# Performance work log

Measured on AMD Instinct MI355X. Metric: run time of the kernel, lower is better.

Reference implementation:

```python
import jax, jax.numpy as jnp
import numpy as np

HEADS = 8

def _rotate_every_two(t):
    # t: [..., d]; interleaved rotation (-x2, x1) pairs
    x1 = t[..., ::2]
    x2 = t[..., 1::2]
    return jnp.stack([-x2, x1], axis=-1).reshape(t.shape)

def _theta_shift(t, sin, cos):
    return t * cos + _rotate_every_two(t) * sin

def setup_inputs() -> dict:
    key = jax.random.key(0)
    ks = jax.random.split(key, 5)
    B, H, W, C = 4, 40, 40, 512
    dh = C // HEADS
    x = jax.random.normal(ks[0], (B, H, W, C), dtype=jnp.float32)
    sin = jax.random.normal(ks[1], (H, W, dh), dtype=jnp.float32)
    cos = jax.random.normal(ks[2], (H, W, dh), dtype=jnp.float32)
    # 1x1 conv weight [3C, C] (kernel dims squeezed) + bias
    w_qkv = jax.random.normal(ks[3], (3 * C, C), dtype=jnp.float32) * (C ** -0.5)
    b_qkv = jnp.zeros((3 * C,), dtype=jnp.float32)
    return {"x": x, "sin": sin, "cos": cos, "w_qkv": w_qkv, "b_qkv": b_qkv}

def reference(x, sin, cos, w_qkv, b_qkv):
    B, H, W, C = x.shape
    heads = HEADS
    dh = C // heads
    scale = dh ** -0.5
    # 1x1 conv == per-pixel linear projection
    qkv = jnp.einsum('bhwc,oc->bhwo', x, w_qkv) + b_qkv  # [B,H,W,3C]
    q, k, v = jnp.split(qkv, 3, axis=-1)

    def to_heads(t):
        # channel order is (heads, dim_head) per the torch rearrange
        return t.reshape(B, H, W, heads, dh).transpose(0, 3, 1, 2, 4)  # [B,heads,H,W,dh]

    q = _theta_shift(to_heads(q), sin, cos)
    k = _theta_shift(to_heads(k), sin, cos)
    # v is computed but unused downstream in the original module (bug preserved)

    N = H * W
    q = q.reshape(B, heads, N, dh)
    k = k.reshape(B, heads, N, dh)

    attn = jnp.einsum('bhnd,bhmd->bhnm', q, k) * scale  # [B,heads,N,N]
    p = jax.nn.softmax(attn, axis=-1)
    # NOTE: original code does matmul(logist, kfine_heads) — K, not V. Kept faithful.
    out = jnp.einsum('bhnm,bhmd->bhnd', p, k)  # [B,heads,N,dh]
    out = out.transpose(0, 2, 1, 3).reshape(B, H, W, C)
    return out
```

## Files before the change

### kernel.cpp

```cpp
#include <hip/hip_runtime.h>
#include <hip/hip_bf16.h>


typedef __hip_bfloat16 bf16;
typedef __attribute__((ext_vector_type(8))) short short8;
typedef __attribute__((ext_vector_type(4))) short bfx4;
typedef __attribute__((ext_vector_type(4))) float f32x4;

#define NSP 1600
#define CDIM 512
#define DH 64

#define GLD16(g, l)                                                           \
  __builtin_amdgcn_global_load_lds(                                           \
      (const __attribute__((address_space(1))) unsigned int*)(g),             \
      (__attribute__((address_space(3))) unsigned int*)(l), 16, 0, 0)

__device__ __forceinline__ f32x4 mfma32(short8 a, short8 b, f32x4 c) {
  return __builtin_amdgcn_mfma_f32_16x16x32_bf16(a, b, c, 0, 0, 0);
}

#if __has_builtin(__builtin_amdgcn_mfma_f32_16x16x16bf16_1k)
__device__ __forceinline__ f32x4 mfma_k16(bfx4 a, bfx4 b, f32x4 c) {
  return __builtin_amdgcn_mfma_f32_16x16x16bf16_1k(a, b, c, 0, 0, 0);
}
#else
__device__ __forceinline__ f32x4 mfma_k16(bfx4 a, bfx4 b, f32x4 c) {
  short8 a8 = {a.x, a.y, a.z, a.w, 0, 0, 0, 0};
  short8 b8 = {b.x, b.y, b.z, b.w, 0, 0, 0, 0};
  return __builtin_amdgcn_mfma_f32_16x16x32_bf16(a8, b8, c, 0, 0, 0);
}
#endif

__device__ __forceinline__ short8 cvt8(float4 v0, float4 v1) {
  short8 r; bf16* p = (bf16*)&r;
  p[0] = __float2bfloat16(v0.x); p[1] = __float2bfloat16(v0.y);
  p[2] = __float2bfloat16(v0.z); p[3] = __float2bfloat16(v0.w);
  p[4] = __float2bfloat16(v1.x); p[5] = __float2bfloat16(v1.y);
  p[6] = __float2bfloat16(v1.z); p[7] = __float2bfloat16(v1.w);
  return r;
}

extern "C" __global__ __launch_bounds__(256)
void cvt_kernel(const float* __restrict__ x, const float* __restrict__ w,
                const float* __restrict__ sin_t, const float* __restrict__ cos_t,
                bf16* __restrict__ x_bf, bf16* __restrict__ w_bf,
                float* __restrict__ sinT, float* __restrict__ cosT)
{
  __shared__ float t_lds[64][68];
  const int bid = blockIdx.x, tid = threadIdx.x;
  if (bid < 1600) {
    const size_t i = (size_t)bid * 2048 + tid * 8;
    float4 v0 = *(const float4*)(x + i);
    float4 v1 = *(const float4*)(x + i + 4);
    *(short8*)(x_bf + i) = cvt8(v0, v1);
  } else if (bid < 1856) {
    const size_t i = (size_t)(bid - 1600) * 2048 + tid * 8;
    float4 v0 = *(const float4*)(w + i);
    float4 v1 = *(const float4*)(w + i + 4);
    *(short8*)(w_bf + i) = cvt8(v0, v1);
  } else {
    const int t = bid - 1856;
    const float* src = (t < 25) ? sin_t : cos_t;
    float* dst = (t < 25) ? sinT : cosT;
    const int nt = (t < 25) ? t : t - 25;
    const int r = tid >> 2, c = (tid & 3) * 16;
#pragma unroll
    for (int j = 0; j < 4; ++j)
      *(float4*)&t_lds[r][c + j * 4] =
          *(const float4*)(src + (size_t)(nt * 64 + r) * 64 + c + j * 4);
    __syncthreads();
#pragma unroll
    for (int j4 = 0; j4 < 4; ++j4) {
      float4 o;
      o.x = t_lds[c + j4 * 4 + 0][r];
      o.y = t_lds[c + j4 * 4 + 1][r];
      o.z = t_lds[c + j4 * 4 + 2][r];
      o.w = t_lds[c + j4 * 4 + 3][r];
      *(float4*)(dst + (size_t)r * NSP + nt * 64 + c + j4 * 4) = o;
    }
  }
}

extern "C" __global__ __launch_bounds__(256)
void proj_kernel(const bf16* __restrict__ x_bf, const bf16* __restrict__ w_bf,
                 const float* __restrict__ bias, const float* __restrict__ sinT,
                 const float* __restrict__ cosT, bf16* __restrict__ q_ws,
                 bf16* __restrict__ k2_ws, bf16* __restrict__ kt2_ws)
{
  __shared__ __align__(16) char smem[65536];
  bf16* ep = (bf16*)smem;

  const int tid  = threadIdx.x;
  const int wave = tid >> 6;
  const int lane = tid & 63;
  const int col  = lane & 15;
  const int quad = lane >> 4;
  const int wm = wave >> 1, wo = wave & 1;
  const int m0 = blockIdx.x * 128;
  const int o0 = blockIdx.y * 128;

  f32x4 acc[4][4];
#pragma unroll
  for (int i = 0; i < 4; ++i)
#pragma unroll
    for (int j = 0; j < 4; ++j) acc[i][j] = {0.f, 0.f, 0.f, 0.f};

  const int rl = lane >> 3;
  const int sck = (lane & 7) ^ rl;
  const int c7 = col & 7;

#define STAGEP(B, KT)                                                         \
  {                                                                           \
    char* xd = smem + (B) * 32768 + wave * 4096;                              \
    char* wd = smem + (B) * 32768 + 16384 + wave * 4096;                      \
    _Pragma("unroll")                                                         \
    for (int i = 0; i < 4; ++i) {                                             \
      const int row = wave * 32 + i * 8 + rl;                                 \
      GLD16(x_bf + ((size_t)(m0 + row) << 9) + (KT) * 64 + sck * 8,           \
            xd + i * 1024);                                                   \
      GLD16(w_bf + ((size_t)(o0 + row) << 9) + (KT) * 64 + sck * 8,           \
            wd + i * 1024);                                                   \
    }                                                                         \
  }

  STAGEP(0, 0)
  __syncthreads();

#pragma unroll
  for (int kt = 0; kt < 8; ++kt) {
    if (kt < 7) { STAGEP((kt + 1) & 1, kt + 1) }
    const char* xls = smem + (kt & 1) * 32768;
    const char* wls = xls + 16384;
#pragma unroll
    for (int half = 0; half < 2; ++half) {
      short8 af[4], bfr[4];
#pragma unroll
      for (int mt = 0; mt < 4; ++mt) {
        const int r = wm * 64 + mt * 16 + col;
        af[mt] = *(const short8*)(xls + r * 128 + (((half * 4 + quad) ^ c7) << 4));
      }
#pragma unroll
      for (int ot = 0; ot < 4; ++ot) {
        const int r = wo * 64 + ot * 16 + col;
        bfr[ot] = *(const short8*)(wls + r * 128 + (((half * 4 + quad) ^ c7) << 4));
      }
#pragma unroll
      for (int mt = 0; mt < 4; ++mt)
#pragma unroll
        for (int ot = 0; ot < 4; ++ot)
          acc[mt][ot] = mfma32(af[mt], bfr[ot], acc[mt][ot]);
    }
    __syncthreads();
  }

  const int b_idx = (m0 + wm * 64) / NSP;
  const int n0w   = m0 + wm * 64 - b_idx * NSP;
  const bool isq  = (o0 < 512);
#pragma unroll
  for (int ot = 0; ot < 4; ++ot) {
    const int o_local = wo * 64 + ot * 16 + col;
    const int o_g = o0 + o_local;
    const float bv = bias[o_g];
    const int d = o_g & 63;
#pragma unroll
    for (int mt = 0; mt < 4; ++mt) {
      const int nl = mt * 16 + quad * 4;
      float t[4], rot[4];
#pragma unroll
      for (int r = 0; r < 4; ++r) t[r] = acc[mt][ot][r] + bv;
#pragma unroll
      for (int r = 0; r < 4; ++r) {
        float tp = __shfl_xor(t[r], 1, 64);
        rot[r] = (lane & 1) ? tp : -tp;
      }
      const float4 c4 = *(const float4*)(cosT + (size_t)d * NSP + n0w + nl);
      const float4 s4 = *(const float4*)(sinT + (size_t)d * NSP + n0w + nl);
      float res[4];
      res[0] = t[0] * c4.x + rot[0] * s4.x;
      res[1] = t[1] * c4.y + rot[1] * s4.y;
      res[2] = t[2] * c4.z + rot[2] * s4.z;
      res[3] = t[3] * c4.w + rot[3] * s4.w;
      if (isq) {
#pragma unroll
        for (int r = 0; r < 4; ++r) res[r] *= 0.125f;
      }
      bfx4 pk; bf16* pp = (bf16*)&pk;
#pragma unroll
      for (int r = 0; r < 4; ++r) pp[r] = __float2bfloat16(res[r]);
      *(bfx4*)&ep[o_local * 132 + wm * 64 + nl] = pk;
    }
  }
  __syncthreads();

  if (isq) {
    const int m_l = tid >> 1, half = tid & 1;
    const int gm = m0 + m_l;
    const int bi = gm / NSP, n = gm - bi * NSP;
    const int h = (o0 >> 6) + half;
    bf16* base = q_ws + ((size_t)(bi * 8 + h) * NSP + n) * 64;
#pragma unroll
    for (int c = 0; c < 8; ++c) {
      short8 v; bf16* vp = (bf16*)&v;
#pragma unroll
      for (int j = 0; j < 8; ++j) vp[j] = ep[(half * 64 + c * 8 + j) * 132 + m_l];
      *(short8*)(base + c * 8) = v;
    }
  } else {
    const int h0 = (o0 - 512) >> 6;
#pragma unroll
    for (int it = 0; it < 8; ++it) {
      const int ci = it * 256 + tid;
      const int hh = ci >> 10, T = (ci >> 9) & 1, inner = ci & 511;
      const int ccol = inner & 15, cq = (inner >> 4) & 3;
      const int f = (inner >> 6) & 1, ti = (inner >> 7) & 1, kh2 = (inner >> 8) & 1;
      const int gmb = m0 + T * 64;
      const int bi = gmb / NSP, ktile = (gmb - bi * NSP) >> 6;
      const int m_l = T * 64 + (2 * kh2 + ti) * 16 + ccol;
      const int er0 = hh * 64 + (f * 4 + cq) * 8;
      short8 v; bf16* vp = (bf16*)&v;
#pragma unroll
      for (int j = 0; j < 8; ++j) vp[j] = ep[(er0 + j) * 132 + m_l];
      *(short8*)(k2_ws +
          (((size_t)(bi * 8 + h0 + hh) * 25 + ktile) * 512 + inner) * 8) = v;
    }
#pragma unroll
    for (int it = 0; it < 8; ++it) {
      const int ci = it * 256 + tid;
      const int hh = ci >> 10, T = (ci >> 9) & 1, inner = ci & 511;
      const int ccol = inner & 15, cq = (inner >> 4) & 3;
      const int dt = (inner >> 6) & 3, kh2 = (inner >> 8) & 1;
      const int gmb = m0 + T * 64;
      const int bi = gmb / NSP, ktile = (gmb - bi * NSP) >> 6;
      const bf16* eprow =
          ep + (hh * 64 + dt * 16 + ccol) * 132 + T * 64 + kh2 * 32 + cq * 4;
      short8 v;
      ((bfx4*)&v)[0] = *(const bfx4*)(eprow);
      ((bfx4*)&v)[1] = *(const bfx4*)(eprow + 16);
      *(short8*)(kt2_ws +
          (((size_t)(bi * 8 + h0 + hh) * 25 + ktile) * 512 + inner) * 8) = v;
    }
  }
}


#define LOADF(KF, KTF, KT)                                                    \
  {                                                                           \
    const bf16* kc_  = k2b  + (KT) * 4096;                                    \
    const bf16* kc2_ = kt2b + (KT) * 4096;                                    \
    _Pragma("unroll")                                                         \
    for (int ti = 0; ti < 2; ++ti)                                            \
      _Pragma("unroll")                                                       \
      for (int f = 0; f < 2; ++f)                                             \
        KF[ti][f] =                                                           \
            *(const short8*)(kc_ + (((kh * 2 + ti) * 2 + f) * 64 + lane) * 8);\
    _Pragma("unroll")                                                         \
    for (int dt = 0; dt < 4; ++dt)                                            \
      KTF[dt] = *(const short8*)(kc2_ + ((kh * 4 + dt) * 64 + lane) * 8);     \
  }

#define COMPUTEF(KF, KTF)                                                     \
  {                                                                           \
    f32x4 s[2][2];                                                            \
    _Pragma("unroll")                                                         \
    for (int ti = 0; ti < 2; ++ti)                                            \
      _Pragma("unroll")                                                       \
      for (int ct = 0; ct < 2; ++ct) {                                        \
        f32x4 t = {0.f, 0.f, 0.f, 0.f};                                       \
        t = mfma32(KF[ti][0], qb[ct][0], t);                                  \
        t = mfma32(KF[ti][1], qb[ct][1], t);                                  \
        s[ti][ct] = t;                                                        \
      }                                                                       \
    bfx4 p4[2][2];                                                            \
    _Pragma("unroll")                                                         \
    for (int ti = 0; ti < 2; ++ti)                                            \
      _Pragma("unroll")                                                       \
      for (int ct = 0; ct < 2; ++ct) {                                        \
        _Pragma("unroll")                                                     \
        for (int r = 0; r < 4; ++r) s[ti][ct][r] = __expf(s[ti][ct][r]);      \
        l_part[ct] +=                                                         \
            s[ti][ct][0] + s[ti][ct][1] + s[ti][ct][2] + s[ti][ct][3];        \
        bf16* pp = (bf16*)&p4[ti][ct];                                        \
        _Pragma("unroll")                                                     \
        for (int r = 0; r < 4; ++r) pp[r] = __float2bfloat16(s[ti][ct][r]);   \
      }                                                                       \
    _Pragma("unroll")                                                         \
    for (int dt = 0; dt < 4; ++dt) {                                          \
      bfx4 alo = __builtin_shufflevector(KTF[dt], KTF[dt], 0, 1, 2, 3);       \
      bfx4 ahi = __builtin_shufflevector(KTF[dt], KTF[dt], 4, 5, 6, 7);       \
      _Pragma("unroll")                                                       \
      for (int ct = 0; ct < 2; ++ct) {                                        \
        oacc[dt][ct] = mfma_k16(alo, p4[0][ct], oacc[dt][ct]);                \
        oacc[dt][ct] = mfma_k16(ahi, p4[1][ct], oacc[dt][ct]);                \
      }                                                                       \
    }                                                                         \
  }

extern "C" __global__ __launch_bounds__(256, 2)
void attn_kernel(const bf16* __restrict__ q_ws, const bf16* __restrict__ k2_ws,
                 const bf16* __restrict__ kt2_ws, float* __restrict__ out)
{
  __shared__ float red[2][64][36];

  const int id = blockIdx.x;
  const int xr = id & 7, inner = id >> 3;
  const int qt = inner % 25;
  const int bh = (inner / 25) * 8 + xr;
  const int b = bh >> 3, h = bh & 7;
  const int tid  = threadIdx.x;
  const int wave = tid >> 6;
  const int lane = tid & 63;
  const int col  = lane & 15;
  const int quad = lane >> 4;
  const int qg = wave & 1, kh = wave >> 1;

  short8 qb[2][2];
#pragma unroll
  for (int ct = 0; ct < 2; ++ct) {
    const bf16* qp =
        q_ws + ((size_t)bh * NSP + qt * 64 + (qg * 2 + ct) * 16 + col) * 64;
    qb[ct][0] = *(const short8*)(qp + quad * 8);
    qb[ct][1] = *(const short8*)(qp + 32 + quad * 8);
  }

  f32x4 oacc[4][2];
#pragma unroll
  for (int i = 0; i < 4; ++i)
#pragma unroll
    for (int j = 0; j < 2; ++j) oacc[i][j] = {0.f, 0.f, 0.f, 0.f};
  float l_part[2] = {0.f, 0.f};

  const bf16* k2b  = k2_ws  + (size_t)bh * 25 * 4096;
  const bf16* kt2b = kt2_ws + (size_t)bh * 25 * 4096;

  short8 kfA[2][2], ktfA[4], kfB[2][2], ktfB[4];
  LOADF(kfA, ktfA, 0)
#pragma unroll 1
  for (int i = 0; i < 12; ++i) {
    LOADF(kfB, ktfB, 2 * i + 1)
    COMPUTEF(kfA, ktfA)
    LOADF(kfA, ktfA, 2 * i + 2)
    COMPUTEF(kfB, ktfB)
  }
  COMPUTEF(kfA, ktfA)

#pragma unroll
  for (int ct = 0; ct < 2; ++ct) {
    l_part[ct] += __shfl_xor(l_part[ct], 16, 64);
    l_part[ct] += __shfl_xor(l_part[ct], 32, 64);
  }

  if (wave >= 2) {
    float* dst = &red[wave - 2][lane][0];
#pragma unroll
    for (int dt = 0; dt < 4; ++dt)
#pragma unroll
      for (int ct = 0; ct < 2; ++ct)
        *(f32x4*)(dst + (dt * 2 + ct) * 4) = oacc[dt][ct];
    dst[32] = l_part[0]; dst[33] = l_part[1];
  }
  __syncthreads();
  if (wave < 2) {
    const float* srcr = &red[wave][lane][0];
#pragma unroll
    for (int dt = 0; dt < 4; ++dt)
#pragma unroll
      for (int ct = 0; ct < 2; ++ct)
        oacc[dt][ct] += *(const f32x4*)(srcr + (dt * 2 + ct) * 4);
    const float inv0 = 1.f / (l_part[0] + srcr[32]);
    const float inv1 = 1.f / (l_part[1] + srcr[33]);
#pragma unroll
    for (int ct = 0; ct < 2; ++ct) {
      const float inv = ct ? inv1 : inv0;
      const int qrow = qt * 64 + (qg * 2 + ct) * 16 + col;
      float* ob = out + ((size_t)b * NSP + qrow) * CDIM + h * 64;
#pragma unroll
      for (int dt = 0; dt < 4; ++dt) {
        float4 v;
        v.x = oacc[dt][ct][0] * inv; v.y = oacc[dt][ct][1] * inv;
        v.z = oacc[dt][ct][2] * inv; v.w = oacc[dt][ct][3] * inv;
        *(float4*)(ob + dt * 16 + quad * 4) = v;
      }
    }
  }
}

extern "C" void kernel_launch(void* const* d_in, const int* in_sizes, int n_in,
                              void* d_out, int out_size, void* d_ws, size_t ws_size,
                              hipStream_t stream) {
  const float* x     = (const float*)d_in[0];
  const float* sin_t = (const float*)d_in[1];
  const float* cos_t = (const float*)d_in[2];
  const float* w_qkv = (const float*)d_in[3];
  const float* b_qkv = (const float*)d_in[4];
  float* out = (float*)d_out;

  const size_t QK = (size_t)32 * NSP * DH;
  bf16* q_ws   = (bf16*)d_ws;
  bf16* k2_ws  = q_ws + QK;
  bf16* kt2_ws = k2_ws + QK;
  bf16* x_bf   = kt2_ws + QK;
  bf16* w_bf   = x_bf + (size_t)6400 * CDIM;
  float* sinT  = (float*)(w_bf + (size_t)1024 * CDIM);
  float* cosT  = sinT + (size_t)DH * NSP;

  cvt_kernel<<<1906, 256, 0, stream>>>(x, w_qkv, sin_t, cos_t, x_bf, w_bf, sinT, cosT);

  dim3 gproj(50, 8);
  proj_kernel<<<gproj, 256, 0, stream>>>(x_bf, w_bf, b_qkv, sinT, cosT,
                                         q_ws, k2_ws, kt2_ws);

  attn_kernel<<<800, 256, 0, stream>>>(q_ws, k2_ws, kt2_ws, out);
}
```

Baseline: 132.2 us.

## Stage K tiles through double-buffered LDS with async global-to-LDS loads

Before, each wave loaded its K and K-transposed fragments straight from global memory into a pair of register buffers. Waves that share the same key half read the same tile, so those global loads were duplicated. The kernel now copies each 16KB K tile once per block into one of two LDS buffers using global_load_lds, prefetching the next tile while the current one is computed. It then reads the fragments from LDS. This halves redundant global/L2 traffic, at the cost of a block-wide barrier every tile, extra LDS reads, and a 32KB LDS footprint that is reused afterwards for the reduction scratch.

```diff
diff --git a/kernel.cpp b/kernel.cpp
--- a/kernel.cpp
+++ b/kernel.cpp
@@ -244,19 +244,30 @@
 }
 
 
-#define LOADF(KF, KTF, KT)                                                    \
+#define ASTAGE(B, KT)                                                         \
   {                                                                           \
-    const bf16* kc_  = k2b  + (KT) * 4096;                                    \
-    const bf16* kc2_ = kt2b + (KT) * 4096;                                    \
+    const char* gk = (const char*)(k2b  + (size_t)(KT) * 4096);               \
+    const char* gt = (const char*)(kt2b + (size_t)(KT) * 4096);               \
+    char* dk = smem + (B) * 16384 + wave * 2048;                              \
+    _Pragma("unroll")                                                         \
+    for (int j = 0; j < 2; ++j) {                                             \
+      GLD16(gk + (wave * 2 + j) * 1024 + lane * 16, dk + j * 1024);           \
+      GLD16(gt + (wave * 2 + j) * 1024 + lane * 16, dk + 8192 + j * 1024);    \
+    }                                                                         \
+  }
+
+#define LOADF_L(KF, KTF, CUR)                                                 \
+  {                                                                           \
+    const char* kl = smem + (CUR) * 16384;                                    \
     _Pragma("unroll")                                                         \
     for (int ti = 0; ti < 2; ++ti)                                            \
       _Pragma("unroll")                                                       \
       for (int f = 0; f < 2; ++f)                                             \
         KF[ti][f] =                                                           \
-            *(const short8*)(kc_ + (((kh * 2 + ti) * 2 + f) * 64 + lane) * 8);\
+            *(const short8*)(kl + (((kh * 2 + ti) * 2 + f) * 64 + lane) * 16);\
     _Pragma("unroll")                                                         \
     for (int dt = 0; dt < 4; ++dt)                                            \
-      KTF[dt] = *(const short8*)(kc2_ + ((kh * 4 + dt) * 64 + lane) * 8);     \
+      KTF[dt] = *(const short8*)(kl + 8192 + ((kh * 4 + dt) * 64 + lane) * 16);\
   }
 
 #define COMPUTEF(KF, KTF)                                                     \
@@ -300,7 +311,8 @@
 void attn_kernel(const bf16* __restrict__ q_ws, const bf16* __restrict__ k2_ws,
                  const bf16* __restrict__ kt2_ws, float* __restrict__ out)
 {
-  __shared__ float red[2][64][36];
+  __shared__ __align__(16) char smem[32768];
+  float* redp = (float*)smem;
 
   const int id = blockIdx.x;
   const int xr = id & 7, inner = id >> 3;
@@ -333,16 +345,17 @@
   const bf16* k2b  = k2_ws  + (size_t)bh * 25 * 4096;
   const bf16* kt2b = kt2_ws + (size_t)bh * 25 * 4096;
 
-  short8 kfA[2][2], ktfA[4], kfB[2][2], ktfB[4];
-  LOADF(kfA, ktfA, 0)
+  ASTAGE(0, 0)
+  __syncthreads();
+
+  short8 kf[2][2], ktf[4];
 #pragma unroll 1
-  for (int i = 0; i < 12; ++i) {
-    LOADF(kfB, ktfB, 2 * i + 1)
-    COMPUTEF(kfA, ktfA)
-    LOADF(kfA, ktfA, 2 * i + 2)
-    COMPUTEF(kfB, ktfB)
-  }
-  COMPUTEF(kfA, ktfA)
+  for (int kt = 0; kt < 25; ++kt) {
+    if (kt < 24) { ASTAGE((kt + 1) & 1, kt + 1) }
+    LOADF_L(kf, ktf, kt & 1)
+    COMPUTEF(kf, ktf)
+    __syncthreads();
+  }
 
 #pragma unroll
   for (int ct = 0; ct < 2; ++ct) {
@@ -351,7 +364,7 @@
   }
 
   if (wave >= 2) {
-    float* dst = &red[wave - 2][lane][0];
+    float* dst = redp + ((size_t)(wave - 2) * 64 + lane) * 36;
 #pragma unroll
     for (int dt = 0; dt < 4; ++dt)
 #pragma unroll
@@ -361,7 +374,7 @@
   }
   __syncthreads();
   if (wave < 2) {
-    const float* srcr = &red[wave][lane][0];
+    const float* srcr = redp + ((size_t)wave * 64 + lane) * 36;
 #pragma unroll
     for (int dt = 0; dt < 4; ++dt)
 #pragma unroll
```

After: 134.3 us. No clear change (+1.6%).
